# Optimization experiments

Measured on AMD Instinct MI355X. Metric: run time of the kernel, lower is better.

## Reference

```python
import jax, jax.numpy as jnp
import numpy as np

B, H, W, C = 1, 64, 512, 256
NH, HS, WS = 8, 4, 32
T = HS * WS            # tokens per window = 128
HD = C // NH           # head dim = 32
L = H * W
SCALE = HD ** -0.5
HID = 4 * C            # mlp hidden
EPS = 1e-5


def _ln(x, g, b):
    m = jnp.mean(x, axis=-1, keepdims=True)
    v = jnp.var(x, axis=-1, keepdims=True)
    return (x - m) * jax.lax.rsqrt(v + EPS) * g + b


def setup_inputs() -> dict:
    key = jax.random.key(0)
    ks = jax.random.split(key, 16)
    def rn(k, shape, s=0.02):
        return jax.random.normal(k, shape, jnp.float32) * s
    return {
        "x": jax.random.normal(ks[0], (B, L, C), jnp.float32),
        "pos": jax.random.normal(ks[1], (B, L, 2), jnp.float32),
        "norm1_g": jnp.ones((C,), jnp.float32), "norm1_b": jnp.zeros((C,), jnp.float32),
        "wq": rn(ks[2], (C, C)), "bq": jnp.zeros((C,), jnp.float32),
        "wk": rn(ks[3], (C, C)), "bk": jnp.zeros((C,), jnp.float32),
        "wv": rn(ks[4], (C, C)), "bv": jnp.zeros((C,), jnp.float32),
        "wo": rn(ks[5], (C, C)), "bo": jnp.zeros((C,), jnp.float32),
        "norm2_g": jnp.ones((C,), jnp.float32), "norm2_b": jnp.zeros((C,), jnp.float32),
        "w_fc1": rn(ks[6], (C, HID)), "b_fc1": jnp.zeros((HID,), jnp.float32),
        "w_fc2": rn(ks[7], (HID, C)), "b_fc2": jnp.zeros((C,), jnp.float32),
        # pos_embedding_cart: Conv1d(2->16,k1), BN1d(16) (inference), ReLU, Conv1d(16->NH,k1)
        "pw1": rn(ks[8], (16, 2), 0.1), "pb1": jnp.zeros((16,), jnp.float32),
        "bn_g": jnp.ones((16,), jnp.float32), "bn_b": jnp.zeros((16,), jnp.float32),
        "bn_m": jnp.zeros((16,), jnp.float32), "bn_v": jnp.ones((16,), jnp.float32),
        "pw2": rn(ks[9], (NH, 16), 0.1), "pb2": jnp.zeros((NH,), jnp.float32),
    }


def _to_windows(t):  # [B,L,C] -> [nW, T, C]
    t = t.reshape(B, H // HS, HS, W // WS, WS, C).transpose(0, 1, 3, 2, 4, 5)
    return t.reshape(-1, T, C)


def _to_heads(t):  # [B,L,C] -> [nW, NH, T, HD]
    return _to_windows(t).reshape(-1, T, NH, HD).transpose(0, 2, 1, 3)


def reference(x, pos, norm1_g, norm1_b, wq, bq, wk, bk, wv, bv, wo, bo,
              norm2_g, norm2_b, w_fc1, b_fc1, w_fc2, b_fc2,
              pw1, pb1, bn_g, bn_b, bn_m, bn_v, pw2, pb2):
    shortcut = x
    xn = _ln(x, norm1_g, norm1_b)

    # relative position bias per window via 1x1 conv net (BN in inference mode)
    posw = pos.reshape(B, H // HS, HS, W // WS, WS, 2).transpose(0, 1, 3, 5, 2, 4)
    posw = posw.reshape(-1, 2, T)                               # [nW, 2, T]
    rel = posw[:, :, :, None] - posw[:, :, None, :]             # [nW, 2, T, T]
    h = jnp.einsum('oc,nctu->notu', pw1, rel) + pb1[None, :, None, None]
    h = (h - bn_m[None, :, None, None]) * jax.lax.rsqrt(bn_v + EPS)[None, :, None, None]
    h = h * bn_g[None, :, None, None] + bn_b[None, :, None, None]
    h = jax.nn.relu(h)
    bias = jnp.einsum('oc,nctu->notu', pw2, h) + pb2[None, :, None, None]  # [nW, NH, T, T]

    q = _to_heads(xn @ wq + bq) * SCALE
    k = _to_heads(xn @ wk + bk)
    v = _to_heads(xn @ wv + bv)

    attn = jax.nn.softmax(jnp.einsum('nhtd,nhud->nhtu', q, k) + bias, axis=-1)
    o = jnp.einsum('nhtu,nhud->nhtd', attn, v)                  # [nW, NH, T, HD]
    o = o.transpose(0, 2, 1, 3).reshape(-1, T, C)               # [nW, T, C]
    o = o.reshape(B, H // HS, W // WS, HS, WS, C).transpose(0, 1, 3, 2, 4, 5)
    o = o.reshape(B, L, C) @ wo + bo

    x1 = shortcut + o
    mlp = jax.nn.gelu(_ln(x1, norm2_g, norm2_b) @ w_fc1 + b_fc1, approximate=False) @ w_fc2 + b_fc2
    return x1 + mlp
```

## Files before the change

kernel.cpp:

```cpp
#include <hip/hip_runtime.h>
#include <cstdint>

typedef unsigned short u16;
typedef __bf16 bf16x8 __attribute__((ext_vector_type(8)));
typedef float f32x4 __attribute__((ext_vector_type(4)));

#define LN_EPS 1e-5f
#define SCALE_Q 0.17677669529663689f

__device__ __forceinline__ u16 f2bf(float f) {
    union { float f; unsigned int i; } c; c.f = f;
    unsigned int r = c.i + 0x7FFFu + ((c.i >> 16) & 1u);
    return (u16)(r >> 16);
}
__device__ __forceinline__ unsigned pack2(float hi, float lo) {
    return __builtin_amdgcn_perm(__float_as_uint(hi), __float_as_uint(lo), 0x07060302u);
}
__device__ __forceinline__ void async16(const void* g, void* l) {
    __builtin_amdgcn_global_load_lds(
        (__attribute__((address_space(1))) unsigned int*)(unsigned long long)g,
        (__attribute__((address_space(3))) unsigned int*)l, 16, 0, 0);
}

__global__ void transpose_all(const float* __restrict__ wq, const float* __restrict__ wk,
                              const float* __restrict__ wv, const float* __restrict__ wo,
                              const float* __restrict__ f1, const float* __restrict__ f2,
                              u16* oq, u16* ok, u16* ov, u16* oo, u16* o1, u16* o2) {
    __shared__ float tile[32][33];
    const int b = blockIdx.x;
    const float* In; u16* Out; int R, C, bx, by;
    if (b < 256) {
        const int m = b >> 6, l = b & 63;
        In = m == 0 ? wq : (m == 1 ? wk : (m == 2 ? wv : wo));
        Out = m == 0 ? oq : (m == 1 ? ok : (m == 2 ? ov : oo));
        R = 256; C = 256; bx = (l & 7) * 32; by = (l >> 3) * 32;
    } else if (b < 512) {
        const int l = b - 256; In = f1; Out = o1; R = 256; C = 1024;
        bx = (l & 31) * 32; by = (l >> 5) * 32;
    } else {
        const int l = b - 512; In = f2; Out = o2; R = 1024; C = 256;
        bx = (l & 7) * 32; by = (l >> 3) * 32;
    }
    const int tx = threadIdx.x, ty = threadIdx.y;
    for (int i = 0; i < 32; i += 8)
        tile[ty + i][tx] = In[(size_t)(by + ty + i) * C + bx + tx];
    __syncthreads();
    for (int i = 0; i < 32; i += 8)
        Out[(size_t)(bx + ty + i) * R + by + tx] = f2bf(tile[tx][ty + i]);
}

__global__ __launch_bounds__(256) void ln_k(const float* __restrict__ X, const float* __restrict__ G,
                                            const float* __restrict__ Bt, u16* __restrict__ Y) {
    const int token = blockIdx.x * 4 + (threadIdx.x >> 6);
    const int ln = threadIdx.x & 63;
    const float4 rv = *(const float4*)(X + (size_t)token * 256 + ln * 4);
    float s = rv.x + rv.y + rv.z + rv.w;
    float q = rv.x * rv.x + rv.y * rv.y + rv.z * rv.z + rv.w * rv.w;
    #pragma unroll
    for (int m = 1; m < 64; m <<= 1) { s += __shfl_xor(s, m, 64); q += __shfl_xor(q, m, 64); }
    const float mean = s * (1.f / 256.f);
    const float var  = q * (1.f / 256.f) - mean * mean;
    const float rs   = rsqrtf(var + LN_EPS);
    const float4 gv = *(const float4*)(G + ln * 4);
    const float4 bv = *(const float4*)(Bt + ln * 4);
    ushort4 o;
    o.x = f2bf((rv.x - mean) * rs * gv.x + bv.x);
    o.y = f2bf((rv.y - mean) * rs * gv.y + bv.y);
    o.z = f2bf((rv.z - mean) * rs * gv.z + bv.z);
    o.w = f2bf((rv.w - mean) * rs * gv.w + bv.w);
    *(ushort4*)(Y + (size_t)token * 256 + ln * 4) = o;
}

__global__ __launch_bounds__(256, 2) void gemm_bt(
    const u16* __restrict__ X, const u16* __restrict__ Wt,
    const float* __restrict__ B1, const float* __restrict__ B2, const float* __restrict__ B3,
    const float* __restrict__ Res,
    u16* __restrict__ Ybf, float* __restrict__ Yf,
    int M, int N, int K, int mode) {
    __shared__ alignas(16) u16 sBuf[128 * 128];
    u16* sA = sBuf;
    u16* sB = sBuf + 128 * 64;
    const int tid = threadIdx.x, wv = tid >> 6, ln = tid & 63;
    const int quad = ln >> 4, l16 = ln & 15;
    const int m0 = blockIdx.y * 128, n0 = blockIdx.x * 128;
    const int mw = (wv >> 1) * 64, nw = (wv & 1) * 64;
    const int r8 = ln >> 3;
    const int kbs = (ln & 7) ^ (r8 & 7);
    const f32x4 z4 = {0.f, 0.f, 0.f, 0.f};
    f32x4 acc[4][4];
    #pragma unroll
    for (int i = 0; i < 4; i++)
        #pragma unroll
        for (int j = 0; j < 4; j++) acc[i][j] = z4;

    for (int k0 = 0; k0 < K; k0 += 64) {
        __syncthreads();
        #pragma unroll
        for (int i = 0; i < 4; i++) {
            const int row = wv * 32 + i * 8;
            async16(X  + (size_t)(m0 + row + r8) * K + k0 + kbs * 8, &sA[row * 64]);
            async16(Wt + (size_t)(n0 + row + r8) * K + k0 + kbs * 8, &sB[row * 64]);
        }
        __syncthreads();
        #pragma unroll
        for (int kk = 0; kk < 2; kk++) {
            bf16x8 af[4], bfr[4];
            #pragma unroll
            for (int i = 0; i < 4; i++) {
                const int ra = mw + i * 16 + l16;
                const int b = kk * 4 + quad;
                af[i] = *(const bf16x8*)&sA[ra * 64 + ((b ^ (ra & 7)) * 8)];
            }
            #pragma unroll
            for (int j = 0; j < 4; j++) {
                const int rb = nw + j * 16 + l16;
                const int b = kk * 4 + quad;
                bfr[j] = *(const bf16x8*)&sB[rb * 64 + ((b ^ (rb & 7)) * 8)];
            }
            #pragma unroll
            for (int i = 0; i < 4; i++)
                #pragma unroll
                for (int j = 0; j < 4; j++)
                    acc[i][j] = __builtin_amdgcn_mfma_f32_16x16x32_bf16(af[i], bfr[j], acc[i][j], 0, 0, 0);
        }
    }
    const int seg = n0 >> 8;
    const float* bp = (mode == 4) ? (seg == 0 ? B1 : (seg == 1 ? B2 : B3)) : B1;
    const float sc = (mode == 4 && seg == 0) ? SCALE_Q : 1.f;
    if (mode == 4) {
        __syncthreads();
        #pragma unroll
        for (int j = 0; j < 4; j++) {
            const int col = nw + j * 16 + l16;
            const float bc = bp[(n0 + col) & 255];
            #pragma unroll
            for (int i = 0; i < 4; i++)
                #pragma unroll
                for (int r = 0; r < 4; r++)
                    sBuf[(mw + i * 16 + quad * 4 + r) * 128 + col] = f2bf((acc[i][j][r] + bc) * sc);
        }
        __syncthreads();
        #pragma unroll
        for (int it = 0; it < 8; it++) {
            const int idx = it * 256 + tid;
            const int row = idx >> 4, sg = idx & 15;
            *(uint4*)(Ybf + (size_t)(m0 + row) * N + n0 + sg * 8) = *(const uint4*)&sBuf[row * 128 + sg * 8];
        }
    } else {
        #pragma unroll
        for (int j = 0; j < 4; j++) {
            const int col = n0 + nw + j * 16 + l16;
            const float bc = bp[col];
            #pragma unroll
            for (int i = 0; i < 4; i++) {
                #pragma unroll
                for (int r = 0; r < 4; r++) {
                    const int row = m0 + mw + i * 16 + quad * 4 + r;
                    float v = acc[i][j][r] + bc;
                    if (mode == 2) v += Res[(size_t)row * N + col];
                    Yf[(size_t)row * N + col] = v;
                }
            }
        }
    }
}

__global__ __launch_bounds__(256) void bias_k(
    const float* __restrict__ pos, const float* __restrict__ pw1, const float* __restrict__ pb1,
    const float* __restrict__ bng, const float* __restrict__ bnb, const float* __restrict__ bnm,
    const float* __restrict__ bnv, const float* __restrict__ pw2, u16* __restrict__ Bg) {
    __shared__ float sTa[32 * 128], sTa2[32 * 128];
    __shared__ u16 sW[16 * 32];
    __shared__ alignas(16) u16 sOut[4][8 * 128];
    const int n = blockIdx.x, wh = n >> 4, ww = n & 15;
    const int tid = threadIdx.x, wv = tid >> 6, ln = tid & 63;
    const int quad = ln >> 4, l16 = ln & 15;
    for (int r = 0; r < 16; r++) {
        const int e = tid + r * 256, o = e >> 7, t = e & 127;
        float ta = 0.f, ta2 = 0.f;
        if (o < 16) {
            const int l = (wh * 4 + (t >> 5)) * 512 + ww * 32 + (t & 31);
            const float sv = rsqrtf(bnv[o] + LN_EPS) * bng[o];
            ta = sv * (pw1[o * 2] * pos[l * 2] + pw1[o * 2 + 1] * pos[l * 2 + 1]);
            ta2 = ta + (pb1[o] - bnm[o]) * sv + bnb[o];
        }
        sTa[o * 128 + t] = ta; sTa2[o * 128 + t] = ta2;
    }
    for (int r = 0; r < 2; r++) {
        const int e = tid + r * 256, h = e >> 5, o = e & 31;
        sW[e] = (h < 8 && o < 16) ? f2bf(pw2[h * 16 + o]) : (u16)0;
    }
    __syncthreads();
    const bf16x8 af = *(const bf16x8*)&sW[l16 * 32 + quad * 8];
    float uo[8][8];
    #pragma unroll
    for (int c = 0; c < 8; c++)
        #pragma unroll
        for (int j = 0; j < 8; j++)
            uo[c][j] = sTa[(quad * 8 + j) * 128 + c * 16 + l16];
    const f32x4 z4 = {0.f, 0.f, 0.f, 0.f};
    u16* outb = Bg + (size_t)n * 131072;
    for (int tl = 0; tl < 32; tl++) {
        const int t = wv * 32 + tl;
        float t2[8];
        #pragma unroll
        for (int j = 0; j < 8; j++) t2[j] = sTa2[(quad * 8 + j) * 128 + t];
        #pragma unroll
        for (int c = 0; c < 8; c++) {
            float rl[8];
            #pragma unroll
            for (int j = 0; j < 8; j++) rl[j] = fmaxf(t2[j] - uo[c][j], 0.f);
            union { unsigned u[4]; bf16x8 v; } bb;
            #pragma unroll
            for (int p = 0; p < 4; p++) bb.u[p] = pack2(rl[2 * p + 1], rl[2 * p]);
            const f32x4 cc = __builtin_amdgcn_mfma_f32_16x16x32_bf16(af, bb.v, z4, 0, 0, 0);
            if (quad < 2) {
                #pragma unroll
                for (int r = 0; r < 4; r++)
                    sOut[wv][(quad * 4 + r) * 128 + c * 16 + l16] =
                        (u16)(__float_as_uint(cc[r]) >> 16);
            }
        }
        #pragma unroll
        for (int it = 0; it < 2; it++) {
            const int idx = it * 64 + ln;
            const int h = idx >> 4, u8 = idx & 15;
            *(uint4*)(outb + (size_t)h * 16384 + t * 128 + u8 * 8) = *(const uint4*)&sOut[wv][idx * 8];
        }
    }
}

__global__ __launch_bounds__(256, 2) void attn_k(
    const u16* __restrict__ Qkv, const u16* __restrict__ Bg, u16* __restrict__ Ob) {
    constexpr int SPS = 136;
    __shared__ alignas(16) u16 sQ[128 * 32];
    __shared__ alignas(16) u16 sK[128 * 32];
    __shared__ alignas(16) u16 sVt[32 * 128];
    __shared__ alignas(16) u16 sPB[128 * SPS];

    const int n = blockIdx.x, h = blockIdx.y;
    const int tid = threadIdx.x, wv = tid >> 6, ln = tid & 63;
    const int quad = ln >> 4, l16 = ln & 15;
    const int wh = n >> 4, ww = n & 15;

    {
        const int rw = ln >> 2;
        const int tb = wv * 16 + rw;
        const int kbq = (ln & 3) ^ (rw & 3);
        #pragma unroll
        for (int i = 0; i < 2; i++) {
            const int tt = tb + i * 64;
            const int l = (wh * 4 + (tt >> 5)) * 512 + ww * 32 + (tt & 31);
            const size_t g = (size_t)l * 768 + h * 32 + kbq * 8;
            async16(Qkv + g, &sQ[(wv * 16 + i * 64) * 32]);
            async16(Qkv + g + 256, &sK[(wv * 16 + i * 64) * 32]);
        }
        const u16* bsrc = Bg + (size_t)(n * 8 + h) * 16384;
        #pragma unroll
        for (int rr = 0; rr < 8; rr++)
            async16(bsrc + rr * 2048 + wv * 512 + ln * 8, &sPB[rr * 2048 + wv * 512]);
        const int d8 = ln & 3;
        #pragma unroll
        for (int i = 0; i < 2; i++) {
            const int tt = tb + i * 64;
            const int l = (wh * 4 + (tt >> 5)) * 512 + ww * 32 + (tt & 31);
            const uint4 raw = *(const uint4*)(Qkv + (size_t)l * 768 + 512 + h * 32 + d8 * 8);
            const u16* e = (const u16*)&raw;
            #pragma unroll
            for (int j = 0; j < 8; j++) {
                const int row = d8 * 8 + j;
                sVt[row * 128 + (((tt >> 3) ^ (row & 15)) * 8) + (tt & 7)] = e[j];
            }
        }
    }
    __syncthreads();

    const f32x4 z4 = {0.f, 0.f, 0.f, 0.f};
    f32x4 acc[2][8];
    {
        bf16x8 qf[2], kf[8];
        #pragma unroll
        for (int i = 0; i < 2; i++) {
            const int t = wv * 32 + i * 16 + l16;
            qf[i] = *(const bf16x8*)&sQ[t * 32 + ((quad ^ (t & 3)) * 8)];
        }
        #pragma unroll
        for (int j = 0; j < 8; j++) {
            const int t = j * 16 + l16;
            kf[j] = *(const bf16x8*)&sK[t * 32 + ((quad ^ (t & 3)) * 8)];
        }
        #pragma unroll
        for (int i = 0; i < 2; i++)
            #pragma unroll
            for (int j = 0; j < 8; j++)
                acc[i][j] = __builtin_amdgcn_mfma_f32_16x16x32_bf16(qf[i], kf[j], z4, 0, 0, 0);
    }
    #pragma unroll
    for (int i = 0; i < 2; i++)
        #pragma unroll
        for (int j = 0; j < 8; j++)
            #pragma unroll
            for (int r = 0; r < 4; r++) {
                const int t = wv * 32 + i * 16 + quad * 4 + r;
                const unsigned bu = sPB[t * 128 + j * 16 + l16];
                acc[i][j][r] += __uint_as_float(bu << 16);
            }
    float rinv[2][4];
    #pragma unroll
    for (int i = 0; i < 2; i++) {
        #pragma unroll
        for (int r = 0; r < 4; r++) {
            float mx = acc[i][0][r];
            #pragma unroll
            for (int j = 1; j < 8; j++) mx = fmaxf(mx, acc[i][j][r]);
            #pragma unroll
            for (int m = 1; m < 16; m <<= 1) mx = fmaxf(mx, __shfl_xor(mx, m, 64));
            float sm = 0.f;
            #pragma unroll
            for (int j = 0; j < 8; j++) {
                const float p = __expf(acc[i][j][r] - mx);
                acc[i][j][r] = p;
                sm += p;
            }
            #pragma unroll
            for (int m = 1; m < 16; m <<= 1) sm += __shfl_xor(sm, m, 64);
            rinv[i][r] = 1.f / sm;
        }
    }
    __syncthreads();
    #pragma unroll
    for (int i = 0; i < 2; i++)
        #pragma unroll
        for (int j = 0; j < 8; j++)
            #pragma unroll
            for (int r = 0; r < 4; r++) {
                const int t = wv * 32 + i * 16 + quad * 4 + r;
                sPB[t * SPS + j * 16 + l16] = (u16)(__float_as_uint(acc[i][j][r]) >> 16);
            }
    __syncthreads();
    f32x4 oacc[2][2];
    #pragma unroll
    for (int i = 0; i < 2; i++)
        #pragma unroll
        for (int jd = 0; jd < 2; jd++) oacc[i][jd] = z4;
    #pragma unroll
    for (int ku = 0; ku < 4; ku++) {
        bf16x8 pf[2], vf[2];
        #pragma unroll
        for (int i = 0; i < 2; i++) pf[i] = *(const bf16x8*)&sPB[(wv * 32 + i * 16 + l16) * SPS + ku * 32 + quad * 8];
        #pragma unroll
        for (int jd = 0; jd < 2; jd++) {
            const int rv = jd * 16 + l16;
            const int b = ku * 4 + quad;
            vf[jd] = *(const bf16x8*)&sVt[rv * 128 + ((b ^ (rv & 15)) * 8)];
        }
        #pragma unroll
        for (int i = 0; i < 2; i++)
            #pragma unroll
            for (int jd = 0; jd < 2; jd++)
                oacc[i][jd] = __builtin_amdgcn_mfma_f32_16x16x32_bf16(pf[i], vf[jd], oacc[i][jd], 0, 0, 0);
    }
    #pragma unroll
    for (int i = 0; i < 2; i++)
        #pragma unroll
        for (int jd = 0; jd < 2; jd++)
            #pragma unroll
            for (int r = 0; r < 4; r++) {
                const int t = wv * 32 + i * 16 + quad * 4 + r;
                const int d = jd * 16 + l16;
                const int l = (wh * 4 + (t >> 5)) * 512 + ww * 32 + (t & 31);
                Ob[(size_t)l * 256 + h * 32 + d] = f2bf(oacc[i][jd][r] * rinv[i][r]);
            }
}

__global__ __launch_bounds__(256, 2) void mlp_fused(
    const u16* __restrict__ Xn, const u16* __restrict__ fc1T, const u16* __restrict__ fc2T,
    const float* __restrict__ b1, const float* __restrict__ b2, float* __restrict__ Out) {
    __shared__ alignas(16) u16 sA[64 * 256];
    __shared__ alignas(16) u16 sW0[64 * 128];
    __shared__ alignas(16) u16 sW1[64 * 128];
    __shared__ alignas(16) u16 sH[64 * 128];
    const int tid = threadIdx.x, wv = tid >> 6, ln = tid & 63;
    const int quad = ln >> 4, l16 = ln & 15;
    const int m0 = blockIdx.x * 64;
    const int mw = (wv >> 1) * 32;
    const int nw1 = (wv & 1) * 64;
    const int nw2 = (wv & 1) * 128;

    auto stage_f1 = [&](int c, int kc, u16* buf) {
        #pragma unroll
        for (int rr = 0; rr < 4; rr++) {
            const int r0 = (rr * 4 + wv) * 8;
            const int row = r0 + (ln >> 3);
            const int kb = (ln & 7) ^ (row & 7);
            async16(fc1T + (size_t)(c * 128 + row) * 256 + kc * 64 + kb * 8, &buf[r0 * 64]);
        }
    };
    auto stage_f2 = [&](int c, int kc, u16* buf) {
        #pragma unroll
        for (int rr = 0; rr < 4; rr++) {
            const int r0 = (rr * 4 + wv) * 16;
            const int row = r0 + (ln >> 2);
            const int kb = (ln & 3) ^ (row & 3);
            async16(fc2T + (size_t)row * 1024 + c * 128 + kc * 32 + kb * 8, &buf[r0 * 32]);
        }
    };

    #pragma unroll
    for (int rr = 0; rr < 8; rr++) {
        const int row2 = rr * 8 + wv * 2;
        const int row = row2 + (ln >> 5);
        const int kb = (ln & 31) ^ (row & 7);
        async16(Xn + (size_t)(m0 + row) * 256 + kb * 8, &sA[row2 * 256]);
    }
    stage_f1(0, 0, sW0);

    const f32x4 z4 = {0.f, 0.f, 0.f, 0.f};
    f32x4 acc2[2][8];
    #pragma unroll
    for (int i = 0; i < 2; i++)
        #pragma unroll
        for (int j = 0; j < 8; j++) acc2[i][j] = z4;

    __syncthreads();
    for (int c = 0; c < 8; c++) {
        f32x4 acc1[2][4];
        #pragma unroll
        for (int i = 0; i < 2; i++)
            #pragma unroll
            for (int j = 0; j < 4; j++) acc1[i][j] = z4;
        #pragma unroll
        for (int kc = 0; kc < 4; kc++) {
            u16* cur = (kc & 1) ? sW1 : sW0;
            u16* nxt = (kc & 1) ? sW0 : sW1;
            if (kc < 3) stage_f1(c, kc + 1, nxt);
            #pragma unroll
            for (int kk = 0; kk < 2; kk++) {
                bf16x8 af[2], bfr[4];
                #pragma unroll
                for (int i = 0; i < 2; i++) {
                    const int ra = mw + i * 16 + l16;
                    const int b = kc * 8 + kk * 4 + quad;
                    af[i] = *(const bf16x8*)&sA[ra * 256 + ((b ^ (ra & 7)) * 8)];
                }
                #pragma unroll
                for (int j = 0; j < 4; j++) {
                    const int rb = nw1 + j * 16 + l16;
                    const int b = kk * 4 + quad;
                    bfr[j] = *(const bf16x8*)&cur[rb * 64 + ((b ^ (rb & 7)) * 8)];
                }
                #pragma unroll
                for (int i = 0; i < 2; i++)
                    #pragma unroll
                    for (int j = 0; j < 4; j++)
                        acc1[i][j] = __builtin_amdgcn_mfma_f32_16x16x32_bf16(af[i], bfr[j], acc1[i][j], 0, 0, 0);
            }
            __syncthreads();
        }
        stage_f2(c, 0, sW0);
        #pragma unroll
        for (int j = 0; j < 4; j++) {
            const float bc = b1[c * 128 + nw1 + j * 16 + l16];
            const int col = nw1 + j * 16 + l16;
            const int blk = col >> 3, off = col & 7;
            #pragma unroll
            for (int i = 0; i < 2; i++)
                #pragma unroll
                for (int r = 0; r < 4; r++) {
                    float v = acc1[i][j][r] + bc;
                    const float p = v * v;
                    const float qq = fmaf(p, -0.07135481283f, -1.5957691216f);
                    v = v / (1.f + __expf(v * qq));
                    const int row = mw + i * 16 + quad * 4 + r;
                    sH[row * 128 + ((blk ^ (row & 15)) * 8) + off] = f2bf(v);
                }
        }
        __syncthreads();
        #pragma unroll
        for (int kc = 0; kc < 4; kc++) {
            u16* cur = (kc & 1) ? sW1 : sW0;
            u16* nxt = (kc & 1) ? sW0 : sW1;
            if (kc < 3) stage_f2(c, kc + 1, nxt);
            else if (c < 7) stage_f1(c + 1, 0, nxt);
            bf16x8 pf[2], bfr[8];
            #pragma unroll
            for (int i = 0; i < 2; i++) {
                const int rp = mw + i * 16 + l16;
                const int b = kc * 4 + quad;
                pf[i] = *(const bf16x8*)&sH[rp * 128 + ((b ^ (rp & 15)) * 8)];
            }
            #pragma unroll
            for (int j = 0; j < 8; j++) {
                const int rb = nw2 + j * 16 + l16;
                bfr[j] = *(const bf16x8*)&cur[rb * 32 + ((quad ^ (rb & 3)) * 8)];
            }
            #pragma unroll
            for (int i = 0; i < 2; i++)
                #pragma unroll
                for (int j = 0; j < 8; j++)
                    acc2[i][j] = __builtin_amdgcn_mfma_f32_16x16x32_bf16(pf[i], bfr[j], acc2[i][j], 0, 0, 0);
            __syncthreads();
        }
    }
    #pragma unroll
    for (int j = 0; j < 8; j++) {
        const int col = nw2 + j * 16 + l16;
        const float bc = b2[col];
        #pragma unroll
        for (int i = 0; i < 2; i++)
            #pragma unroll
            for (int r = 0; r < 4; r++) {
                const size_t idx = (size_t)(m0 + mw + i * 16 + quad * 4 + r) * 256 + col;
                Out[idx] = acc2[i][j][r] + bc + Out[idx];
            }
    }
}

extern "C" void kernel_launch(void* const* d_in, const int* in_sizes, int n_in,
                              void* d_out, int out_size, void* d_ws, size_t ws_size,
                              hipStream_t stream) {
    const float* x    = (const float*)d_in[0];
    const float* pos  = (const float*)d_in[1];
    const float* n1g  = (const float*)d_in[2];
    const float* n1b  = (const float*)d_in[3];
    const float* wq   = (const float*)d_in[4];
    const float* bq   = (const float*)d_in[5];
    const float* wk   = (const float*)d_in[6];
    const float* bk   = (const float*)d_in[7];
    const float* wvw  = (const float*)d_in[8];
    const float* bv   = (const float*)d_in[9];
    const float* wo   = (const float*)d_in[10];
    const float* bo   = (const float*)d_in[11];
    const float* n2g  = (const float*)d_in[12];
    const float* n2b  = (const float*)d_in[13];
    const float* wfc1 = (const float*)d_in[14];
    const float* bfc1 = (const float*)d_in[15];
    const float* wfc2 = (const float*)d_in[16];
    const float* bfc2 = (const float*)d_in[17];
    const float* pw1  = (const float*)d_in[18];
    const float* pb1  = (const float*)d_in[19];
    const float* bng  = (const float*)d_in[20];
    const float* bnb  = (const float*)d_in[21];
    const float* bnm  = (const float*)d_in[22];
    const float* bnv  = (const float*)d_in[23];
    const float* pw2  = (const float*)d_in[24];
    float* out = (float*)d_out;
    u16* ws  = (u16*)d_ws;

    const size_t SZ = (size_t)32768 * 256;
    u16* s0   = ws;
    u16* qkv  = ws + SZ;
    u16* wqT  = ws + 4 * SZ;
    u16* wkT  = wqT + 65536;
    u16* wvT  = wkT + 65536;
    u16* woT  = wvT + 65536;
    u16* fc1T = woT + 65536;
    u16* fc2T = fc1T + 262144;
    u16* biasg = fc2T + 262144;

    transpose_all<<<768, dim3(32, 8), 0, stream>>>(wq, wk, wvw, wo, wfc1, wfc2,
                                                   wqT, wkT, wvT, woT, fc1T, fc2T);
    ln_k<<<8192, 256, 0, stream>>>(x, n1g, n1b, s0);
    gemm_bt<<<dim3(6, 256), 256, 0, stream>>>(s0, wqT, bq, bk, bv, nullptr, qkv, nullptr,
                                              32768, 768, 256, 4);
    bias_k<<<256, 256, 0, stream>>>(pos, pw1, pb1, bng, bnb, bnm, bnv, pw2, biasg);
    attn_k<<<dim3(256, 8), 256, 0, stream>>>(qkv, biasg, s0);
    gemm_bt<<<dim3(2, 256), 256, 0, stream>>>(s0, woT, bo, nullptr, nullptr, x, nullptr, out,
                                              32768, 256, 256, 2);
    ln_k<<<8192, 256, 0, stream>>>(out, n2g, n2b, s0);
    mlp_fused<<<512, 256, 0, stream>>>(s0, fc1T, fc2T, bfc1, bfc2, out);
}
```

Baseline: 320.4 us.

## Fuse output projection with residual and LayerNorm2, and merge small prep launches

Adds a wo_ln_k kernel that does the Wo projection with 64-row tiles covering all 256 columns. Its epilogue adds bias and residual, writes the fp32 output, then computes LayerNorm2 through shuffle and LDS reductions and writes bf16 normalized rows. This removes the separate LN2 pass that re-read the fp32 intermediate. It also folds the weight transposes and LN1 into one launch, and the QKV GEMM and the position-bias MLP into another, cutting launch count. The trade-off is a larger LDS footprint and in-place reuse of the s0 buffer, which depends on each block only reading its own rows.

After: 297.4 us. 7.2% less time.

```diff
diff --git a/kernel.cpp b/kernel.cpp
--- a/kernel.cpp
+++ b/kernel.cpp
@@ -22,112 +22,117 @@
         (__attribute__((address_space(3))) unsigned int*)l, 16, 0, 0);
 }
 
-__global__ void transpose_all(const float* __restrict__ wq, const float* __restrict__ wk,
-                              const float* __restrict__ wv, const float* __restrict__ wo,
-                              const float* __restrict__ f1, const float* __restrict__ f2,
-                              u16* oq, u16* ok, u16* ov, u16* oo, u16* o1, u16* o2) {
+__global__ __launch_bounds__(256) void prep_k(
+    const float* __restrict__ wq, const float* __restrict__ wk,
+    const float* __restrict__ wv, const float* __restrict__ wo,
+    const float* __restrict__ f1, const float* __restrict__ f2,
+    u16* oq, u16* ok, u16* ov, u16* oo, u16* o1, u16* o2,
+    const float* __restrict__ X, const float* __restrict__ G,
+    const float* __restrict__ Bt, u16* __restrict__ Y) {
     __shared__ float tile[32][33];
     const int b = blockIdx.x;
-    const float* In; u16* Out; int R, C, bx, by;
-    if (b < 256) {
-        const int m = b >> 6, l = b & 63;
-        In = m == 0 ? wq : (m == 1 ? wk : (m == 2 ? wv : wo));
-        Out = m == 0 ? oq : (m == 1 ? ok : (m == 2 ? ov : oo));
-        R = 256; C = 256; bx = (l & 7) * 32; by = (l >> 3) * 32;
-    } else if (b < 512) {
-        const int l = b - 256; In = f1; Out = o1; R = 256; C = 1024;
-        bx = (l & 31) * 32; by = (l >> 5) * 32;
+    const int tid = threadIdx.x;
+    if (b < 768) {
+        const float* In; u16* Out; int R, C, bx, by;
+        if (b < 256) {
+            const int m = b >> 6, l = b & 63;
+            In = m == 0 ? wq : (m == 1 ? wk : (m == 2 ? wv : wo));
+            Out = m == 0 ? oq : (m == 1 ? ok : (m == 2 ? ov : oo));
+            R = 256; C = 256; bx = (l & 7) * 32; by = (l >> 3) * 32;
+        } else if (b < 512) {
+            const int l = b - 256; In = f1; Out = o1; R = 256; C = 1024;
+            bx = (l & 31) * 32; by = (l >> 5) * 32;
+        } else {
+            const int l = b - 512; In = f2; Out = o2; R = 1024; C = 256;
+            bx = (l & 7) * 32; by = (l >> 3) * 32;
+        }
+        const int tx = tid & 31, ty = tid >> 5;
+        for (int i = 0; i < 32; i += 8)
+            tile[ty + i][tx] = In[(size_t)(by + ty + i) * C + bx + tx];
+        __syncthreads();
+        for (int i = 0; i < 32; i += 8)
+            Out[(size_t)(bx + ty + i) * R + by + tx] = f2bf(tile[tx][ty + i]);
     } else {
-        const int l = b - 512; In = f2; Out = o2; R = 1024; C = 256;
-        bx = (l & 7) * 32; by = (l >> 3) * 32;
-    }
-    const int tx = threadIdx.x, ty = threadIdx.y;
-    for (int i = 0; i < 32; i += 8)
-        tile[ty + i][tx] = In[(size_t)(by + ty + i) * C + bx + tx];
-    __syncthreads();
-    for (int i = 0; i < 32; i += 8)
-        Out[(size_t)(bx + ty + i) * R + by + tx] = f2bf(tile[tx][ty + i]);
-}
-
-__global__ __launch_bounds__(256) void ln_k(const float* __restrict__ X, const float* __restrict__ G,
-                                            const float* __restrict__ Bt, u16* __restrict__ Y) {
-    const int token = blockIdx.x * 4 + (threadIdx.x >> 6);
-    const int ln = threadIdx.x & 63;
-    const float4 rv = *(const float4*)(X + (size_t)token * 256 + ln * 4);
-    float s = rv.x + rv.y + rv.z + rv.w;
-    float q = rv.x * rv.x + rv.y * rv.y + rv.z * rv.z + rv.w * rv.w;
-    #pragma unroll
-    for (int m = 1; m < 64; m <<= 1) { s += __shfl_xor(s, m, 64); q += __shfl_xor(q, m, 64); }
-    const float mean = s * (1.f / 256.f);
-    const float var  = q * (1.f / 256.f) - mean * mean;
-    const float rs   = rsqrtf(var + LN_EPS);
-    const float4 gv = *(const float4*)(G + ln * 4);
-    const float4 bv = *(const float4*)(Bt + ln * 4);
-    ushort4 o;
-    o.x = f2bf((rv.x - mean) * rs * gv.x + bv.x);
-    o.y = f2bf((rv.y - mean) * rs * gv.y + bv.y);
-    o.z = f2bf((rv.z - mean) * rs * gv.z + bv.z);
-    o.w = f2bf((rv.w - mean) * rs * gv.w + bv.w);
-    *(ushort4*)(Y + (size_t)token * 256 + ln * 4) = o;
-}
-
-__global__ __launch_bounds__(256, 2) void gemm_bt(
+        const int token = (b - 768) * 4 + (tid >> 6);
+        const int ln = tid & 63;
+        const float4 rv = *(const float4*)(X + (size_t)token * 256 + ln * 4);
+        float s = rv.x + rv.y + rv.z + rv.w;
+        float q = rv.x * rv.x + rv.y * rv.y + rv.z * rv.z + rv.w * rv.w;
+        #pragma unroll
+        for (int m = 1; m < 64; m <<= 1) { s += __shfl_xor(s, m, 64); q += __shfl_xor(q, m, 64); }
+        const float mean = s * (1.f / 256.f);
+        const float var  = q * (1.f / 256.f) - mean * mean;
+        const float rs   = rsqrtf(var + LN_EPS);
+        const float4 gv = *(const float4*)(G + ln * 4);
+        const float4 bv = *(const float4*)(Bt + ln * 4);
+        ushort4 o;
+        o.x = f2bf((rv.x - mean) * rs * gv.x + bv.x);
+        o.y = f2bf((rv.y - mean) * rs * gv.y + bv.y);
+        o.z = f2bf((rv.z - mean) * rs * gv.z + bv.z);
+        o.w = f2bf((rv.w - mean) * rs * gv.w + bv.w);
+        *(ushort4*)(Y + (size_t)token * 256 + ln * 4) = o;
+    }
+}
+
+__global__ __launch_bounds__(256, 2) void qkvbias_k(
     const u16* __restrict__ X, const u16* __restrict__ Wt,
     const float* __restrict__ B1, const float* __restrict__ B2, const float* __restrict__ B3,
-    const float* __restrict__ Res,
-    u16* __restrict__ Ybf, float* __restrict__ Yf,
-    int M, int N, int K, int mode) {
-    __shared__ alignas(16) u16 sBuf[128 * 128];
-    u16* sA = sBuf;
-    u16* sB = sBuf + 128 * 64;
+    u16* __restrict__ Ybf,
+    const float* __restrict__ pos, const float* __restrict__ pw1, const float* __restrict__ pb1,
+    const float* __restrict__ bng, const float* __restrict__ bnb, const float* __restrict__ bnm,
+    const float* __restrict__ bnv, const float* __restrict__ pw2, u16* __restrict__ Bg) {
+    __shared__ alignas(16) unsigned char raw[42 * 1024];
     const int tid = threadIdx.x, wv = tid >> 6, ln = tid & 63;
     const int quad = ln >> 4, l16 = ln & 15;
-    const int m0 = blockIdx.y * 128, n0 = blockIdx.x * 128;
-    const int mw = (wv >> 1) * 64, nw = (wv & 1) * 64;
-    const int r8 = ln >> 3;
-    const int kbs = (ln & 7) ^ (r8 & 7);
     const f32x4 z4 = {0.f, 0.f, 0.f, 0.f};
-    f32x4 acc[4][4];
-    #pragma unroll
-    for (int i = 0; i < 4; i++)
-        #pragma unroll
-        for (int j = 0; j < 4; j++) acc[i][j] = z4;
-
-    for (int k0 = 0; k0 < K; k0 += 64) {
-        __syncthreads();
-        #pragma unroll
-        for (int i = 0; i < 4; i++) {
-            const int row = wv * 32 + i * 8;
-            async16(X  + (size_t)(m0 + row + r8) * K + k0 + kbs * 8, &sA[row * 64]);
-            async16(Wt + (size_t)(n0 + row + r8) * K + k0 + kbs * 8, &sB[row * 64]);
-        }
-        __syncthreads();
-        #pragma unroll
-        for (int kk = 0; kk < 2; kk++) {
-            bf16x8 af[4], bfr[4];
+    if (blockIdx.x < 1536) {
+        u16* sBuf = (u16*)raw;
+        u16* sA = sBuf;
+        u16* sB = sBuf + 128 * 64;
+        const int n0 = (blockIdx.x % 6) * 128, m0 = (blockIdx.x / 6) * 128;
+        const int K = 256, N = 768;
+        const int mw = (wv >> 1) * 64, nw = (wv & 1) * 64;
+        const int r8 = ln >> 3;
+        const int kbs = (ln & 7) ^ (r8 & 7);
+        f32x4 acc[4][4];
+        #pragma unroll
+        for (int i = 0; i < 4; i++)
+            #pragma unroll
+            for (int j = 0; j < 4; j++) acc[i][j] = z4;
+        for (int k0 = 0; k0 < K; k0 += 64) {
+            __syncthreads();
             #pragma unroll
             for (int i = 0; i < 4; i++) {
-                const int ra = mw + i * 16 + l16;
-                const int b = kk * 4 + quad;
-                af[i] = *(const bf16x8*)&sA[ra * 64 + ((b ^ (ra & 7)) * 8)];
-            }
-            #pragma unroll
-            for (int j = 0; j < 4; j++) {
-                const int rb = nw + j * 16 + l16;
-                const int b = kk * 4 + quad;
-                bfr[j] = *(const bf16x8*)&sB[rb * 64 + ((b ^ (rb & 7)) * 8)];
-            }
-            #pragma unroll
-            for (int i = 0; i < 4; i++)
-                #pragma unroll
-                for (int j = 0; j < 4; j++)
-                    acc[i][j] = __builtin_amdgcn_mfma_f32_16x16x32_bf16(af[i], bfr[j], acc[i][j], 0, 0, 0);
-        }
-    }
-    const int seg = n0 >> 8;
-    const float* bp = (mode == 4) ? (seg == 0 ? B1 : (seg == 1 ? B2 : B3)) : B1;
-    const float sc = (mode == 4 && seg == 0) ? SCALE_Q : 1.f;
-    if (mode == 4) {
+                const int row = wv * 32 + i * 8;
+                async16(X  + (size_t)(m0 + row + r8) * K + k0 + kbs * 8, &sA[row * 64]);
+                async16(Wt + (size_t)(n0 + row + r8) * K + k0 + kbs * 8, &sB[row * 64]);
+            }
+            __syncthreads();
+            #pragma unroll
+            for (int kk = 0; kk < 2; kk++) {
+                bf16x8 af[4], bfr[4];
+                #pragma unroll
+                for (int i = 0; i < 4; i++) {
+                    const int ra = mw + i * 16 + l16;
+                    const int bb = kk * 4 + quad;
+                    af[i] = *(const bf16x8*)&sA[ra * 64 + ((bb ^ (ra & 7)) * 8)];
+                }
+                #pragma unroll
+                for (int j = 0; j < 4; j++) {
+                    const int rb = nw + j * 16 + l16;
+                    const int bb = kk * 4 + quad;
+                    bfr[j] = *(const bf16x8*)&sB[rb * 64 + ((bb ^ (rb & 7)) * 8)];
+                }
+                #pragma unroll
+                for (int i = 0; i < 4; i++)
+                    #pragma unroll
+                    for (int j = 0; j < 4; j++)
+                        acc[i][j] = __builtin_amdgcn_mfma_f32_16x16x32_bf16(af[i], bfr[j], acc[i][j], 0, 0, 0);
+            }
+        }
+        const int seg = n0 >> 8;
+        const float* bp = seg == 0 ? B1 : (seg == 1 ? B2 : B3);
+        const float sc = seg == 0 ? SCALE_Q : 1.f;
         __syncthreads();
         #pragma unroll
         for (int j = 0; j < 4; j++) {
@@ -147,85 +152,62 @@
             *(uint4*)(Ybf + (size_t)(m0 + row) * N + n0 + sg * 8) = *(const uint4*)&sBuf[row * 128 + sg * 8];
         }
     } else {
-        #pragma unroll
-        for (int j = 0; j < 4; j++) {
-            const int col = n0 + nw + j * 16 + l16;
-            const float bc = bp[col];
-            #pragma unroll
-            for (int i = 0; i < 4; i++) {
-                #pragma unroll
-                for (int r = 0; r < 4; r++) {
-                    const int row = m0 + mw + i * 16 + quad * 4 + r;
-                    float v = acc[i][j][r] + bc;
-                    if (mode == 2) v += Res[(size_t)row * N + col];
-                    Yf[(size_t)row * N + col] = v;
+        float* sTa  = (float*)raw;
+        float* sTa2 = sTa + 32 * 128;
+        u16*   sW   = (u16*)(sTa2 + 32 * 128);
+        u16*   sOut = sW + 512;
+        const int n = blockIdx.x - 1536, wh = n >> 4, ww = n & 15;
+        for (int r = 0; r < 16; r++) {
+            const int e = tid + r * 256, o = e >> 7, t = e & 127;
+            float ta = 0.f, ta2 = 0.f;
+            if (o < 16) {
+                const int l = (wh * 4 + (t >> 5)) * 512 + ww * 32 + (t & 31);
+                const float sv = rsqrtf(bnv[o] + LN_EPS) * bng[o];
+                ta = sv * (pw1[o * 2] * pos[l * 2] + pw1[o * 2 + 1] * pos[l * 2 + 1]);
+                ta2 = ta + (pb1[o] - bnm[o]) * sv + bnb[o];
+            }
+            sTa[o * 128 + t] = ta; sTa2[o * 128 + t] = ta2;
+        }
+        for (int r = 0; r < 2; r++) {
+            const int e = tid + r * 256, h = e >> 5, o = e & 31;
+            sW[e] = (h < 8 && o < 16) ? f2bf(pw2[h * 16 + o]) : (u16)0;
+        }
+        __syncthreads();
+        const bf16x8 af = *(const bf16x8*)&sW[l16 * 32 + quad * 8];
+        float uo[8][8];
+        #pragma unroll
+        for (int c = 0; c < 8; c++)
+            #pragma unroll
+            for (int j = 0; j < 8; j++)
+                uo[c][j] = sTa[(quad * 8 + j) * 128 + c * 16 + l16];
+        u16* outb = Bg + (size_t)n * 131072;
+        for (int tl = 0; tl < 32; tl++) {
+            const int t = wv * 32 + tl;
+            float t2[8];
+            #pragma unroll
+            for (int j = 0; j < 8; j++) t2[j] = sTa2[(quad * 8 + j) * 128 + t];
+            #pragma unroll
+            for (int c = 0; c < 8; c++) {
+                float rl[8];
+                #pragma unroll
+                for (int j = 0; j < 8; j++) rl[j] = fmaxf(t2[j] - uo[c][j], 0.f);
+                union { unsigned u[4]; bf16x8 v; } bb;
+                #pragma unroll
+                for (int p = 0; p < 4; p++) bb.u[p] = pack2(rl[2 * p + 1], rl[2 * p]);
+                const f32x4 cc = __builtin_amdgcn_mfma_f32_16x16x32_bf16(af, bb.v, z4, 0, 0, 0);
+                if (quad < 2) {
+                    #pragma unroll
+                    for (int r = 0; r < 4; r++)
+                        sOut[wv * 1024 + (quad * 4 + r) * 128 + c * 16 + l16] =
+                            (u16)(__float_as_uint(cc[r]) >> 16);
                 }
             }
-        }
-    }
-}
-
-__global__ __launch_bounds__(256) void bias_k(
-    const float* __restrict__ pos, const float* __restrict__ pw1, const float* __restrict__ pb1,
-    const float* __restrict__ bng, const float* __restrict__ bnb, const float* __restrict__ bnm,
-    const float* __restrict__ bnv, const float* __restrict__ pw2, u16* __restrict__ Bg) {
-    __shared__ float sTa[32 * 128], sTa2[32 * 128];
-    __shared__ u16 sW[16 * 32];
-    __shared__ alignas(16) u16 sOut[4][8 * 128];
-    const int n = blockIdx.x, wh = n >> 4, ww = n & 15;
-    const int tid = threadIdx.x, wv = tid >> 6, ln = tid & 63;
-    const int quad = ln >> 4, l16 = ln & 15;
-    for (int r = 0; r < 16; r++) {
-        const int e = tid + r * 256, o = e >> 7, t = e & 127;
-        float ta = 0.f, ta2 = 0.f;
-        if (o < 16) {
-            const int l = (wh * 4 + (t >> 5)) * 512 + ww * 32 + (t & 31);
-            const float sv = rsqrtf(bnv[o] + LN_EPS) * bng[o];
-            ta = sv * (pw1[o * 2] * pos[l * 2] + pw1[o * 2 + 1] * pos[l * 2 + 1]);
-            ta2 = ta + (pb1[o] - bnm[o]) * sv + bnb[o];
-        }
-        sTa[o * 128 + t] = ta; sTa2[o * 128 + t] = ta2;
-    }
-    for (int r = 0; r < 2; r++) {
-        const int e = tid + r * 256, h = e >> 5, o = e & 31;
-        sW[e] = (h < 8 && o < 16) ? f2bf(pw2[h * 16 + o]) : (u16)0;
-    }
-    __syncthreads();
-    const bf16x8 af = *(const bf16x8*)&sW[l16 * 32 + quad * 8];
-    float uo[8][8];
-    #pragma unroll
-    for (int c = 0; c < 8; c++)
-        #pragma unroll
-        for (int j = 0; j < 8; j++)
-            uo[c][j] = sTa[(quad * 8 + j) * 128 + c * 16 + l16];
-    const f32x4 z4 = {0.f, 0.f, 0.f, 0.f};
-    u16* outb = Bg + (size_t)n * 131072;
-    for (int tl = 0; tl < 32; tl++) {
-        const int t = wv * 32 + tl;
-        float t2[8];
-        #pragma unroll
-        for (int j = 0; j < 8; j++) t2[j] = sTa2[(quad * 8 + j) * 128 + t];
-        #pragma unroll
-        for (int c = 0; c < 8; c++) {
-            float rl[8];
-            #pragma unroll
-            for (int j = 0; j < 8; j++) rl[j] = fmaxf(t2[j] - uo[c][j], 0.f);
-            union { unsigned u[4]; bf16x8 v; } bb;
-            #pragma unroll
-            for (int p = 0; p < 4; p++) bb.u[p] = pack2(rl[2 * p + 1], rl[2 * p]);
-            const f32x4 cc = __builtin_amdgcn_mfma_f32_16x16x32_bf16(af, bb.v, z4, 0, 0, 0);
-            if (quad < 2) {
-                #pragma unroll
-                for (int r = 0; r < 4; r++)
-                    sOut[wv][(quad * 4 + r) * 128 + c * 16 + l16] =
-                        (u16)(__float_as_uint(cc[r]) >> 16);
-            }
-        }
-        #pragma unroll
-        for (int it = 0; it < 2; it++) {
-            const int idx = it * 64 + ln;
-            const int h = idx >> 4, u8 = idx & 15;
-            *(uint4*)(outb + (size_t)h * 16384 + t * 128 + u8 * 8) = *(const uint4*)&sOut[wv][idx * 8];
+            #pragma unroll
+            for (int it = 0; it < 2; it++) {
+                const int idx = it * 64 + ln;
+                const int h = idx >> 4, u8 = idx & 15;
+                *(uint4*)(outb + (size_t)h * 16384 + t * 128 + u8 * 8) = *(const uint4*)&sOut[wv * 1024 + idx * 8];
+            }
         }
     }
 }
@@ -264,8 +246,8 @@
         for (int i = 0; i < 2; i++) {
             const int tt = tb + i * 64;
             const int l = (wh * 4 + (tt >> 5)) * 512 + ww * 32 + (tt & 31);
-            const uint4 raw = *(const uint4*)(Qkv + (size_t)l * 768 + 512 + h * 32 + d8 * 8);
-            const u16* e = (const u16*)&raw;
+            const uint4 rawv = *(const uint4*)(Qkv + (size_t)l * 768 + 512 + h * 32 + d8 * 8);
+            const u16* e = (const u16*)&rawv;
             #pragma unroll
             for (int j = 0; j < 8; j++) {
                 const int row = d8 * 8 + j;
@@ -371,6 +353,131 @@
                 const int l = (wh * 4 + (t >> 5)) * 512 + ww * 32 + (t & 31);
                 Ob[(size_t)l * 256 + h * 32 + d] = f2bf(oacc[i][jd][r] * rinv[i][r]);
             }
+}
+
+__global__ __launch_bounds__(256, 2) void wo_ln_k(
+    const u16* __restrict__ O, const u16* __restrict__ woT, const float* __restrict__ bo,
+    const float* __restrict__ x, const float* __restrict__ n2g, const float* __restrict__ n2b,
+    float* __restrict__ out, u16* __restrict__ xn2) {
+    __shared__ alignas(16) u16 sA[64 * 64];
+    __shared__ alignas(16) u16 sB[256 * 64];
+    __shared__ float sRed[64 * 4];
+    const int tid = threadIdx.x, wv = tid >> 6, ln = tid & 63;
+    const int quad = ln >> 4, l16 = ln & 15;
+    const int m0 = blockIdx.x * 64;
+    const int mw = (wv >> 1) * 32, nw = (wv & 1) * 128;
+    const f32x4 z4 = {0.f, 0.f, 0.f, 0.f};
+    f32x4 acc[2][8];
+    #pragma unroll
+    for (int i = 0; i < 2; i++)
+        #pragma unroll
+        for (int j = 0; j < 8; j++) acc[i][j] = z4;
+
+    for (int k0 = 0; k0 < 256; k0 += 64) {
+        __syncthreads();
+        #pragma unroll
+        for (int r = 0; r < 2; r++) {
+            const int row = r * 32 + wv * 8 + (ln >> 3);
+            const int kb = (ln & 7) ^ (row & 7);
+            async16(O + (size_t)(m0 + row) * 256 + k0 + kb * 8, &sA[(r * 32 + wv * 8) * 64]);
+        }
+        #pragma unroll
+        for (int r = 0; r < 8; r++) {
+            const int row = r * 32 + wv * 8 + (ln >> 3);
+            const int kb = (ln & 7) ^ (row & 7);
+            async16(woT + (size_t)row * 256 + k0 + kb * 8, &sB[(r * 32 + wv * 8) * 64]);
+        }
+        __syncthreads();
+        #pragma unroll
+        for (int kk = 0; kk < 2; kk++) {
+            bf16x8 af[2], bfr[8];
+            #pragma unroll
+            for (int i = 0; i < 2; i++) {
+                const int ra = mw + i * 16 + l16;
+                const int b = kk * 4 + quad;
+                af[i] = *(const bf16x8*)&sA[ra * 64 + ((b ^ (ra & 7)) * 8)];
+            }
+            #pragma unroll
+            for (int j = 0; j < 8; j++) {
+                const int rb = nw + j * 16 + l16;
+                const int b = kk * 4 + quad;
+                bfr[j] = *(const bf16x8*)&sB[rb * 64 + ((b ^ (rb & 7)) * 8)];
+            }
+            #pragma unroll
+            for (int i = 0; i < 2; i++)
+                #pragma unroll
+                for (int j = 0; j < 8; j++)
+                    acc[i][j] = __builtin_amdgcn_mfma_f32_16x16x32_bf16(af[i], bfr[j], acc[i][j], 0, 0, 0);
+        }
+    }
+    float s[2][4], q[2][4];
+    #pragma unroll
+    for (int i = 0; i < 2; i++)
+        #pragma unroll
+        for (int r = 0; r < 4; r++) { s[i][r] = 0.f; q[i][r] = 0.f; }
+    #pragma unroll
+    for (int j = 0; j < 8; j++) {
+        const int col = nw + j * 16 + l16;
+        const float bc = bo[col];
+        #pragma unroll
+        for (int i = 0; i < 2; i++)
+            #pragma unroll
+            for (int r = 0; r < 4; r++) {
+                const int row = mw + i * 16 + quad * 4 + r;
+                const size_t idx = (size_t)(m0 + row) * 256 + col;
+                const float v = acc[i][j][r] + bc + x[idx];
+                out[idx] = v;
+                acc[i][j][r] = v;
+                s[i][r] += v; q[i][r] += v * v;
+            }
+    }
+    #pragma unroll
+    for (int i = 0; i < 2; i++)
+        #pragma unroll
+        for (int r = 0; r < 4; r++) {
+            #pragma unroll
+            for (int m = 1; m < 16; m <<= 1) {
+                s[i][r] += __shfl_xor(s[i][r], m, 64);
+                q[i][r] += __shfl_xor(q[i][r], m, 64);
+            }
+        }
+    __syncthreads();
+    if (l16 == 0) {
+        #pragma unroll
+        for (int i = 0; i < 2; i++)
+            #pragma unroll
+            for (int r = 0; r < 4; r++) {
+                const int row = mw + i * 16 + quad * 4 + r;
+                sRed[row * 4 + (wv & 1) * 2]     = s[i][r];
+                sRed[row * 4 + (wv & 1) * 2 + 1] = q[i][r];
+            }
+    }
+    __syncthreads();
+    float mean[2][4], rsv[2][4];
+    #pragma unroll
+    for (int i = 0; i < 2; i++)
+        #pragma unroll
+        for (int r = 0; r < 4; r++) {
+            const int row = mw + i * 16 + quad * 4 + r;
+            const float S = sRed[row * 4] + sRed[row * 4 + 2];
+            const float Q = sRed[row * 4 + 1] + sRed[row * 4 + 3];
+            const float mn = S * (1.f / 256.f);
+            mean[i][r] = mn;
+            rsv[i][r] = rsqrtf(Q * (1.f / 256.f) - mn * mn + LN_EPS);
+        }
+    #pragma unroll
+    for (int j = 0; j < 8; j++) {
+        const int col = nw + j * 16 + l16;
+        const float g = n2g[col], bb = n2b[col];
+        #pragma unroll
+        for (int i = 0; i < 2; i++)
+            #pragma unroll
+            for (int r = 0; r < 4; r++) {
+                const int row = mw + i * 16 + quad * 4 + r;
+                xn2[(size_t)(m0 + row) * 256 + col] =
+                    f2bf((acc[i][j][r] - mean[i][r]) * rsv[i][r] * g + bb);
+            }
+    }
 }
 
 __global__ __launch_bounds__(256, 2) void mlp_fused(
@@ -558,15 +665,12 @@
     u16* fc2T = fc1T + 262144;
     u16* biasg = fc2T + 262144;
 
-    transpose_all<<<768, dim3(32, 8), 0, stream>>>(wq, wk, wvw, wo, wfc1, wfc2,
-                                                   wqT, wkT, wvT, woT, fc1T, fc2T);
-    ln_k<<<8192, 256, 0, stream>>>(x, n1g, n1b, s0);
-    gemm_bt<<<dim3(6, 256), 256, 0, stream>>>(s0, wqT, bq, bk, bv, nullptr, qkv, nullptr,
-                                              32768, 768, 256, 4);
-    bias_k<<<256, 256, 0, stream>>>(pos, pw1, pb1, bng, bnb, bnm, bnv, pw2, biasg);
+    prep_k<<<8960, 256, 0, stream>>>(wq, wk, wvw, wo, wfc1, wfc2,
+                                     wqT, wkT, wvT, woT, fc1T, fc2T,
+                                     x, n1g, n1b, s0);
+    qkvbias_k<<<1792, 256, 0, stream>>>(s0, wqT, bq, bk, bv, qkv,
+                                        pos, pw1, pb1, bng, bnb, bnm, bnv, pw2, biasg);
     attn_k<<<dim3(256, 8), 256, 0, stream>>>(qkv, biasg, s0);
-    gemm_bt<<<dim3(2, 256), 256, 0, stream>>>(s0, woT, bo, nullptr, nullptr, x, nullptr, out,
-                                              32768, 256, 256, 2);
-    ln_k<<<8192, 256, 0, stream>>>(out, n2g, n2b, s0);
+    wo_ln_k<<<512, 256, 0, stream>>>(s0, woT, bo, x, n2g, n2b, out, s0);
     mlp_fused<<<512, 256, 0, stream>>>(s0, fc1T, fc2T, bfc1, bfc2, out);
 }
```
